# Kernel tuning notes

Measured on AMD Instinct MI355X. Metric: run time of the kernel, lower is better.

## Reference

```python
import jax, jax.numpy as jnp
import numpy as np

KM_ITERS = 20  # fixed Lloyd iterations (scipy kmeans iterates to tolerance with random init;
               # we use deterministic min/max init so centroid 0 = dark, 1 = bright)


def _kmeans_mask(img2d):
    """2-means clustering of pixel intensities of one [H,W] image + border-vote flip."""
    H, W = img2d.shape
    x = img2d.reshape(-1)  # [N]
    c0 = jnp.stack([x.min(), x.max()])  # deterministic init: centroid0=min, centroid1=max

    def step(c, _):
        code = jnp.argmin(jnp.abs(x[:, None] - c[None, :]), axis=1)  # [N] in {0,1}
        one = code == 1
        n1 = jnp.sum(one)
        n0 = x.shape[0] - n1
        s1 = jnp.sum(jnp.where(one, x, jnp.zeros_like(x)))
        s0 = jnp.sum(x) - s1
        c_new = jnp.stack([s0 / jnp.maximum(n0, 1).astype(x.dtype),
                           s1 / jnp.maximum(n1, 1).astype(x.dtype)])
        return c_new, None

    c, _ = jax.lax.scan(step, c0, None, length=KM_ITERS)
    # final assignment (scipy vq step)
    code = jnp.argmin(jnp.abs(x[:, None] - c[None, :]), axis=1).reshape(H, W)

    # border vote: if >=3 borders are mostly cluster-1, flip so text region is 1
    fc = code[:, 0].sum()
    lc = code[:, -1].sum()
    fr = code[0, :].sum()
    lr = code[-1, :].sum()
    num = ((fr > W // 2).astype(jnp.int32) + (lr > W // 2).astype(jnp.int32)
           + (fc > H // 2).astype(jnp.int32) + (lc > H // 2).astype(jnp.int32))
    mask = jnp.where(num >= 3, 1 - code, code)
    return mask.astype(img2d.dtype)


def get_mask(img_tensor):
    gray = img_tensor.mean(axis=1)  # [B,H,W]
    # clustering is non-differentiable in the original (runs on detached CPU numpy)
    masks = jax.vmap(_kmeans_mask)(jax.lax.stop_gradient(gray))
    return masks[:, None, :, :]  # [B,1,H,W]


def setup_inputs() -> dict:
    key = jax.random.key(0)
    k1, k2 = jax.random.split(key)
    B, C, H, W = 128, 3, 256, 256
    hr_img = jax.random.uniform(k1, (B, C, H, W), dtype=jnp.float32)
    sr_mask = jax.random.uniform(k2, (B, 1, H, W), dtype=jnp.float32)
    return {"hr_img": hr_img, "sr_mask": sr_mask}


def reference(hr_img, sr_mask):
    hr_mask = get_mask(hr_img)  # same spatial size -> no interpolation branch
    return jnp.mean((sr_mask - hr_mask) ** 2)
```

## Files before the change

### kernel.cpp

```cpp
#include <hip/hip_runtime.h>


constexpr int NB   = 2048;
constexpr int NPIX = 65536;
constexpr int KM_ITERS = 20;
constexpr float QINV = 1.0f / 65536.0f;
constexpr float BINW = 1.0f / 2048.0f;
constexpr unsigned CNT1   = 1u << 19;
constexpr unsigned SVMASK = CNT1 - 1;

constexpr size_t OFF_HIST = 0;
constexpr size_t OFF_MMN  = 1048576;
constexpr size_t OFF_MMX  = OFF_MMN + 4096;
constexpr size_t OFF_SR2  = OFF_MMX + 4096;
constexpr size_t OFF_ACC  = OFF_SR2 + 4096;
constexpr size_t OFF_BG   = OFF_ACC + 4096;
constexpr size_t MEMSET_BYTES = 1048576;

__device__ __forceinline__ float waveSumF(float v) {
#pragma unroll
    for (int off = 32; off > 0; off >>= 1) v += __shfl_down(v, off, 64);
    return v;
}
__device__ __forceinline__ unsigned waveMinU(unsigned v) {
#pragma unroll
    for (int off = 32; off > 0; off >>= 1) v = min(v, (unsigned)__shfl_down((int)v, off, 64));
    return v;
}
__device__ __forceinline__ unsigned waveMaxU(unsigned v) {
#pragma unroll
    for (int off = 32; off > 0; off >>= 1) v = max(v, (unsigned)__shfl_down((int)v, off, 64));
    return v;
}

__global__ __launch_bounds__(512) void kA_hist(
        const float* __restrict__ hr, const float* __restrict__ sr,
        unsigned* __restrict__ hist,
        unsigned* __restrict__ mmn, unsigned* __restrict__ mmx,
        float* __restrict__ bsr2, ushort* __restrict__ bg,
        float* __restrict__ acc, unsigned* __restrict__ done) {
    const int blk = blockIdx.x, img = blk >> 3, part = blk & 7;
    const int tid = threadIdx.x, lane = tid & 63, wid = tid >> 6;

    __shared__ unsigned hc[NB];
    __shared__ unsigned smn[8], smx[8];
    __shared__ float    ssq[8];
    for (int j = tid; j < NB; j += 512) hc[j] = 0u;
    if (blk == 0 && tid == 0) { *acc = 0.0f; *done = 0u; }
    __syncthreads();

    const float* rr = hr + (size_t)img * 3 * NPIX;
    const float* gg = rr + NPIX;
    const float* bb = gg + NPIX;
    const float* sp = sr + (size_t)img * NPIX;
    ushort* bgp = bg + (size_t)img * 1024;

    unsigned umn = 65535u, umx = 0u;
    float sq = 0.0f;
#pragma unroll
    for (int i = 0; i < 4; ++i) {
        const int p = part * 8192 + i * 2048 + tid * 4;
        float4 r4 = *(const float4*)(rr + p);
        float4 g4 = *(const float4*)(gg + p);
        float4 b4 = *(const float4*)(bb + p);
        float4 s4 = *(const float4*)(sp + p);
        const float x[4] = { (r4.x + g4.x + b4.x) * (1.0f / 3.0f),
                             (r4.y + g4.y + b4.y) * (1.0f / 3.0f),
                             (r4.z + g4.z + b4.z) * (1.0f / 3.0f),
                             (r4.w + g4.w + b4.w) * (1.0f / 3.0f) };
        const float sv[4] = { s4.x, s4.y, s4.z, s4.w };
        unsigned u[4];
#pragma unroll
        for (int j = 0; j < 4; ++j) {
            unsigned uu = (unsigned)(x[j] * 65536.0f);
            uu = min(uu, 65535u);
            u[j] = uu;
            umn = min(umn, uu); umx = max(umx, uu);
            unsigned q = (unsigned)(sv[j] * 64.0f + 0.5f);
            q = min(q, 63u);
            atomicAdd(&hc[uu >> 5], CNT1 + q);
            sq += sv[j] * sv[j];
        }
        const int row = p >> 8, colb = p & 255;
        if (row == 0) {
            ushort4 qq; qq.x = (ushort)u[0]; qq.y = (ushort)u[1];
            qq.z = (ushort)u[2]; qq.w = (ushort)u[3];
            *(ushort4*)(bgp + colb) = qq;
        }
        if (row == 255) {
            ushort4 qq; qq.x = (ushort)u[0]; qq.y = (ushort)u[1];
            qq.z = (ushort)u[2]; qq.w = (ushort)u[3];
            *(ushort4*)(bgp + 256 + colb) = qq;
        }
        if (colb == 0)   bgp[512 + row] = (ushort)u[0];
        if (colb == 252) bgp[768 + row] = (ushort)u[3];
    }
    __syncthreads();

    unsigned* gh = hist + (size_t)img * NB;
    for (int j = tid; j < NB; j += 512) {
        const unsigned v = hc[j];
        if (v) atomicAdd(&gh[j], v);
    }

    sq = waveSumF(sq); umn = waveMinU(umn); umx = waveMaxU(umx);
    if (lane == 0) { ssq[wid] = sq; smn[wid] = umn; smx[wid] = umx; }
    __syncthreads();
    if (tid == 0) {
        float SQ = 0.0f; unsigned MN = 65535u, MX = 0u;
#pragma unroll
        for (int w = 0; w < 8; ++w) {
            SQ += ssq[w]; MN = min(MN, smn[w]); MX = max(MX, smx[w]);
        }
        bsr2[blk] = SQ; mmn[blk] = MN; mmx[blk] = MX;
    }
}

__global__ __launch_bounds__(256) void kB_all(
        const unsigned* __restrict__ mmn, const unsigned* __restrict__ mmx,
        const float* __restrict__ bsr2, const ushort* __restrict__ bg,
        const unsigned* __restrict__ hist,
        float* __restrict__ acc, unsigned* __restrict__ done,
        float* __restrict__ out) {
    const int img = blockIdx.x, tid = threadIdx.x;
    const int lane = tid & 63, wid = tid >> 6;
    __shared__ float sN[NB + 1], sS[NB + 1], sV[NB + 1];
    __shared__ float tN[256], tS[256], tV[256];
    __shared__ float bres[4];
    __shared__ float4 sB4[4];

    const int base = tid * 8;
    const unsigned* gh = hist + (size_t)img * NB + base;
    const uint4 p0 = *(const uint4*)gh;
    const uint4 p1 = *(const uint4*)(gh + 4);
    const unsigned pk[8] = { p0.x, p0.y, p0.z, p0.w, p1.x, p1.y, p1.z, p1.w };
    float n8[8], s8[8], v8[8];
#pragma unroll
    for (int u = 0; u < 8; ++u) {
        const float c = (float)(pk[u] >> 19);
        n8[u] = c;
        s8[u] = c * (((float)(base + u) + 0.484375f) * BINW);
        v8[u] = (float)(pk[u] & SVMASK) * (1.0f / 64.0f);
    }

    float accN = 0.0f, accS = 0.0f, accV = 0.0f;
#pragma unroll
    for (int u = 7; u >= 0; --u) {
        accN += n8[u]; n8[u] = accN;
        accS += s8[u]; s8[u] = accS;
        accV += v8[u]; v8[u] = accV;
    }
    tN[tid] = accN; tS[tid] = accS; tV[tid] = accV;
    __syncthreads();
    for (int off = 1; off < 256; off <<= 1) {
        float aNN = 0.0f, aSS = 0.0f, aVV = 0.0f;
        if (tid + off < 256) { aNN = tN[tid + off]; aSS = tS[tid + off]; aVV = tV[tid + off]; }
        __syncthreads();
        tN[tid] += aNN; tS[tid] += aSS; tV[tid] += aVV;
        __syncthreads();
    }
    const float exN = (tid < 255) ? tN[tid + 1] : 0.0f;
    const float exS = (tid < 255) ? tS[tid + 1] : 0.0f;
    const float exV = (tid < 255) ? tV[tid + 1] : 0.0f;
#pragma unroll
    for (int u = 0; u < 8; ++u) {
        sN[base + u] = n8[u] + exN;
        sS[base + u] = s8[u] + exS;
        sV[base + u] = v8[u] + exV;
    }
    if (tid == 0) { sN[NB] = 0.0f; sS[NB] = 0.0f; sV[NB] = 0.0f; }
    __syncthreads();

    if (tid == 0) {
        unsigned bmn = 65535u, bmx = 0u;
#pragma unroll
        for (int s = 0; s < 8; ++s) {
            bmn = min(bmn, mmn[img * 8 + s]);
            bmx = max(bmx, mmx[img * 8 + s]);
        }
        float c0f = (float)bmn * QINV;
        float c1f = (float)bmx * QINV;
        const float Stot = sS[0];
        const float Ntot = (float)NPIX;
#pragma unroll 1
        for (int it = 0; it < KM_ITERS; ++it) {
            const float t = 0.5f * (c0f + c1f);
            float n1, s1;
            if (c1f == c0f) { n1 = 0.0f; s1 = 0.0f; }
            else {
                const float f = t * (float)NB;
                int k = (int)floorf(f);
                k = max(0, min(NB - 1, k));
                float frac = (float)(k + 1) - f;
                frac = fminf(fmaxf(frac, 0.0f), 1.0f);
                const float cntk = sN[k] - sN[k + 1];
                const float aNt = sN[k + 1] + cntk * frac;
                const float aSt = sS[k + 1] +
                                  cntk * frac * 0.5f * (t + (float)(k + 1) * BINW);
                if (c1f > c0f) { n1 = aNt; s1 = aSt; }
                else           { n1 = Ntot - aNt; s1 = Stot - aSt; }
            }
            const float c1n = s1 / fmaxf(n1, 1.0f);
            const float c0n = (Stot - s1) / fmaxf(Ntot - n1, 1.0f);
            if (c1n == c1f && c0n == c0f) break;
            c0f = c0n; c1f = c1n;
        }

        float Sr2 = 0.0f;
#pragma unroll
        for (int s = 0; s < 8; ++s) Sr2 += bsr2[img * 8 + s];
        const float SvTot = sV[0];

        float tf, hii, n1, s1v;
        if (c1f == c0f) { tf = -1e30f; hii = 0.0f; n1 = 0.0f; s1v = 0.0f; }
        else {
            tf = 0.5f * (c0f + c1f);
            const float f = tf * (float)NB;
            int k = (int)floorf(f);
            k = max(0, min(NB - 1, k));
            float frac = (float)(k + 1) - f;
            frac = fminf(fmaxf(frac, 0.0f), 1.0f);
            const float cntk = sN[k] - sN[k + 1];
            const float aNt = sN[k + 1] + cntk * frac;
            const float svk = sV[k] - sV[k + 1];
            const float aSv = sV[k + 1] + svk * frac;
            if (c1f > c0f) { hii = 1.0f; n1 = aNt;        s1v = aSv; }
            else           { hii = 0.0f; n1 = Ntot - aNt; s1v = SvTot - aSv; }
        }
        bres[0] = tf; bres[1] = hii;
        bres[2] = Sr2 - 2.0f * s1v + n1;
        bres[3] = Sr2 - 2.0f * (SvTot - s1v) + (Ntot - n1);
    }
    __syncthreads();

    const float tf = bres[0];
    const bool hi = (bres[1] != 0.0f);
    const ushort* bp = bg + (size_t)img * 1024;
    const float x0 = (float)bp[tid]       * QINV;
    const float x1 = (float)bp[256 + tid] * QINV;
    const float x2 = (float)bp[512 + tid] * QINV;
    const float x3 = (float)bp[768 + tid] * QINV;
    float fr = (hi ? (x0 > tf) : (x0 < tf)) ? 1.0f : 0.0f;
    float lr = (hi ? (x1 > tf) : (x1 < tf)) ? 1.0f : 0.0f;
    float fc = (hi ? (x2 > tf) : (x2 < tf)) ? 1.0f : 0.0f;
    float lc = (hi ? (x3 > tf) : (x3 < tf)) ? 1.0f : 0.0f;
    fr = waveSumF(fr); lr = waveSumF(lr); fc = waveSumF(fc); lc = waveSumF(lc);
    if (lane == 0) sB4[wid] = make_float4(fr, lr, fc, lc);
    __syncthreads();
    if (tid == 0) {
        const float FR = sB4[0].x + sB4[1].x + sB4[2].x + sB4[3].x;
        const float LR = sB4[0].y + sB4[1].y + sB4[2].y + sB4[3].y;
        const float FC = sB4[0].z + sB4[1].z + sB4[2].z + sB4[3].z;
        const float LC = sB4[0].w + sB4[1].w + sB4[2].w + sB4[3].w;
        const int num = (FR > 128.0f) + (LR > 128.0f) + (FC > 128.0f) + (LC > 128.0f);
        const float chosen = (num >= 3) ? bres[3] : bres[2];
        atomicAdd(acc, chosen);
        __threadfence();
        const unsigned old = atomicAdd(done, 1u);
        if (old == 127u) {
            const float tot = atomicAdd(acc, 0.0f);
            out[0] = tot * (1.0f / 8388608.0f);
        }
    }
}

extern "C" void kernel_launch(void* const* d_in, const int* in_sizes, int n_in,
                              void* d_out, int out_size, void* d_ws, size_t ws_size,
                              hipStream_t stream) {
    const float* hr = (const float*)d_in[0];
    const float* sr = (const float*)d_in[1];
    float* out = (float*)d_out;

    char* ws = (char*)d_ws;
    unsigned* hist = (unsigned*)(ws + OFF_HIST);
    unsigned* mmn  = (unsigned*)(ws + OFF_MMN);
    unsigned* mmx  = (unsigned*)(ws + OFF_MMX);
    float*    bsr2 = (float*)(ws + OFF_SR2);
    float*    acc  = (float*)(ws + OFF_ACC);
    unsigned* done = (unsigned*)(ws + OFF_ACC + 4);
    ushort*   bg   = (ushort*)(ws + OFF_BG);

    hipMemsetAsync(hist, 0, MEMSET_BYTES, stream);
    kA_hist<<<1024, 512, 0, stream>>>(hr, sr, hist, mmn, mmx, bsr2, bg, acc, done);
    kB_all <<< 128, 256, 0, stream>>>(mmn, mmx, bsr2, bg, hist, acc, done, out);
}
```

Before: 184.4 us.

## Split histogram pass into LDS-privatized and global-atomic kernels by image half

The histogram kernel is split in two. Images 0-63 keep the shared-memory privatized histogram, and images 64-127 go to a new kernel that does atomic adds straight into the global histogram without LDS. The apparent aim is to balance LDS atomic pressure against L2 atomic throughput, or to probe which path is faster. The trade-off is one extra launch, serialization between the two kernels on the same stream, and heavy global atomic contention for half the images.

```diff
diff --git a/kernel.cpp b/kernel.cpp
--- a/kernel.cpp
+++ b/kernel.cpp
@@ -33,7 +33,25 @@
     return v;
 }
 
-__global__ __launch_bounds__(512) void kA_hist(
+__device__ __forceinline__ void blockTail(
+        int blk, int tid, int lane, int wid, float sq, unsigned umn, unsigned umx,
+        unsigned* smn, unsigned* smx, float* ssq,
+        unsigned* __restrict__ mmn, unsigned* __restrict__ mmx,
+        float* __restrict__ bsr2) {
+    sq = waveSumF(sq); umn = waveMinU(umn); umx = waveMaxU(umx);
+    if (lane == 0) { ssq[wid] = sq; smn[wid] = umn; smx[wid] = umx; }
+    __syncthreads();
+    if (tid == 0) {
+        float SQ = 0.0f; unsigned MN = 65535u, MX = 0u;
+#pragma unroll
+        for (int w = 0; w < 8; ++w) {
+            SQ += ssq[w]; MN = min(MN, smn[w]); MX = max(MX, smx[w]);
+        }
+        bsr2[blk] = SQ; mmn[blk] = MN; mmx[blk] = MX;
+    }
+}
+
+__global__ __launch_bounds__(512) void kA_lds(
         const float* __restrict__ hr, const float* __restrict__ sr,
         unsigned* __restrict__ hist,
         unsigned* __restrict__ mmn, unsigned* __restrict__ mmx,
@@ -55,11 +73,12 @@
     const float* sp = sr + (size_t)img * NPIX;
     ushort* bgp = bg + (size_t)img * 1024;
 
+    const int p0 = part * 8192 + tid * 4;
     unsigned umn = 65535u, umx = 0u;
     float sq = 0.0f;
 #pragma unroll
     for (int i = 0; i < 4; ++i) {
-        const int p = part * 8192 + i * 2048 + tid * 4;
+        const int p = p0 + i * 2048;
         float4 r4 = *(const float4*)(rr + p);
         float4 g4 = *(const float4*)(gg + p);
         float4 b4 = *(const float4*)(bb + p);
@@ -102,18 +121,71 @@
         const unsigned v = hc[j];
         if (v) atomicAdd(&gh[j], v);
     }
-
-    sq = waveSumF(sq); umn = waveMinU(umn); umx = waveMaxU(umx);
-    if (lane == 0) { ssq[wid] = sq; smn[wid] = umn; smx[wid] = umx; }
-    __syncthreads();
-    if (tid == 0) {
-        float SQ = 0.0f; unsigned MN = 65535u, MX = 0u;
-#pragma unroll
-        for (int w = 0; w < 8; ++w) {
-            SQ += ssq[w]; MN = min(MN, smn[w]); MX = max(MX, smx[w]);
-        }
-        bsr2[blk] = SQ; mmn[blk] = MN; mmx[blk] = MX;
-    }
+    blockTail(blk, tid, lane, wid, sq, umn, umx, smn, smx, ssq, mmn, mmx, bsr2);
+}
+
+__global__ __launch_bounds__(512) void kA_glb(
+        const float* __restrict__ hr, const float* __restrict__ sr,
+        unsigned* __restrict__ hist,
+        unsigned* __restrict__ mmn, unsigned* __restrict__ mmx,
+        float* __restrict__ bsr2, ushort* __restrict__ bg) {
+    const int img = 64 + (blockIdx.x >> 3), part = blockIdx.x & 7;
+    const int blk = img * 8 + part;
+    const int tid = threadIdx.x, lane = tid & 63, wid = tid >> 6;
+
+    __shared__ unsigned smn[8], smx[8];
+    __shared__ float    ssq[8];
+
+    const float* rr = hr + (size_t)img * 3 * NPIX;
+    const float* gg = rr + NPIX;
+    const float* bb = gg + NPIX;
+    const float* sp = sr + (size_t)img * NPIX;
+    ushort* bgp = bg + (size_t)img * 1024;
+    unsigned* gh = hist + (size_t)img * NB;
+
+    const int p0 = part * 8192 + tid * 4;
+    unsigned umn = 65535u, umx = 0u;
+    float sq = 0.0f;
+#pragma unroll
+    for (int i = 0; i < 4; ++i) {
+        const int p = p0 + i * 2048;
+        float4 r4 = *(const float4*)(rr + p);
+        float4 g4 = *(const float4*)(gg + p);
+        float4 b4 = *(const float4*)(bb + p);
+        float4 s4 = *(const float4*)(sp + p);
+        const float x[4] = { (r4.x + g4.x + b4.x) * (1.0f / 3.0f),
+                             (r4.y + g4.y + b4.y) * (1.0f / 3.0f),
+                             (r4.z + g4.z + b4.z) * (1.0f / 3.0f),
+                             (r4.w + g4.w + b4.w) * (1.0f / 3.0f) };
+        const float sv[4] = { s4.x, s4.y, s4.z, s4.w };
+        unsigned u[4];
+#pragma unroll
+        for (int j = 0; j < 4; ++j) {
+            unsigned uu = (unsigned)(x[j] * 65536.0f);
+            uu = min(uu, 65535u);
+            u[j] = uu;
+            umn = min(umn, uu); umx = max(umx, uu);
+            unsigned q = (unsigned)(sv[j] * 64.0f + 0.5f);
+            q = min(q, 63u);
+            atomicAdd(&gh[uu >> 5], CNT1 + q);
+            sq += sv[j] * sv[j];
+        }
+        const int row = p >> 8, colb = p & 255;
+        if (row == 0) {
+            ushort4 qq; qq.x = (ushort)u[0]; qq.y = (ushort)u[1];
+            qq.z = (ushort)u[2]; qq.w = (ushort)u[3];
+            *(ushort4*)(bgp + colb) = qq;
+        }
+        if (row == 255) {
+            ushort4 qq; qq.x = (ushort)u[0]; qq.y = (ushort)u[1];
+            qq.z = (ushort)u[2]; qq.w = (ushort)u[3];
+            *(ushort4*)(bgp + 256 + colb) = qq;
+        }
+        if (colb == 0)   bgp[512 + row] = (ushort)u[0];
+        if (colb == 252) bgp[768 + row] = (ushort)u[3];
+    }
+    __syncthreads();
+    blockTail(blk, tid, lane, wid, sq, umn, umx, smn, smx, ssq, mmn, mmx, bsr2);
 }
 
 __global__ __launch_bounds__(256) void kB_all(
@@ -281,6 +353,7 @@
     ushort*   bg   = (ushort*)(ws + OFF_BG);
 
     hipMemsetAsync(hist, 0, MEMSET_BYTES, stream);
-    kA_hist<<<1024, 512, 0, stream>>>(hr, sr, hist, mmn, mmx, bsr2, bg, acc, done);
-    kB_all <<< 128, 256, 0, stream>>>(mmn, mmx, bsr2, bg, hist, acc, done, out);
-}
+    kA_lds<<<512, 512, 0, stream>>>(hr, sr, hist, mmn, mmx, bsr2, bg, acc, done);
+    kA_glb<<<512, 512, 0, stream>>>(hr, sr, hist, mmn, mmx, bsr2, bg);
+    kB_all<<<128, 256, 0, stream>>>(mmn, mmx, bsr2, bg, hist, acc, done, out);
+}
```

Result: slower. 315.7 us (+71.2%).
